# Kernel tuning notes

Measured on AMD Instinct MI355X. Metric: run time of the kernel, lower is better.

The kernel has to match this reference:

```python
import jax, jax.numpy as jnp
import numpy as np

S, B, D, H, DH = 2048, 2, 1024, 16, 64


def setup_inputs() -> dict:
    key = jax.random.key(0)
    ks = jax.random.split(key, 7)
    sc = 0.02
    return {
        "x": jax.random.normal(ks[0], (S, B, D), jnp.float32),
        "pos_emb": jax.random.normal(ks[1], (S, D), jnp.float32),
        "pos_bias_u": jax.random.normal(ks[2], (H, DH), jnp.float32) * sc,
        "pos_bias_v": jax.random.normal(ks[3], (H, DH), jnp.float32) * sc,
        "W_qkv": jax.random.normal(ks[4], (D, 3 * H * DH), jnp.float32) * sc,
        "W_relemb": jax.random.normal(ks[5], (D, H * DH), jnp.float32) * sc,
        "W_o": jax.random.normal(ks[6], (H * DH, D), jnp.float32) * sc,
        "ln_gamma": jnp.ones((D,), jnp.float32),
        "ln_beta": jnp.zeros((D,), jnp.float32),
    }


def _rel_shift(x):
    # x: [i, j, b, n]; Transformer-XL relative shift
    i, j, b, n = x.shape
    zero_pad = jnp.zeros((i, 1, b, n), x.dtype)
    xp = jnp.concatenate([zero_pad, x], axis=1)      # [i, j+1, b, n]
    xp = xp.reshape(j + 1, i, b, n)
    return xp[1:].reshape(i, j, b, n)


def reference(x, pos_emb, pos_bias_u, pos_bias_v, W_qkv, W_relemb, W_o, ln_gamma, ln_beta):
    seq_len, batch, d_model = x.shape
    num_head, d_head = pos_bias_u.shape
    scale = jnp.asarray(1.0 / d_head ** 0.5, x.dtype)

    qkv = x @ W_qkv                                   # [S,B,3*H*DH]
    q, k, v = jnp.split(qkv, 3, axis=-1)
    q = q.reshape(seq_len, batch, num_head, d_head)
    k = k.reshape(seq_len, batch, num_head, d_head)
    v = v.reshape(seq_len, batch, num_head, d_head)
    r = (pos_emb @ W_relemb).reshape(seq_len, num_head, d_head)

    AC = jnp.einsum('ibnd,jbnd->ijbn', q + pos_bias_u, k)
    BD = _rel_shift(jnp.einsum('ibnd,jnd->ijbn', q + pos_bias_v, r))
    attn_score = (AC + BD) * scale                    # [S,S,B,H]
    attn_prob = jax.nn.softmax(attn_score, axis=1)

    attn_vec = jnp.einsum('ijbn,jbnd->ibnd', attn_prob, v)
    attn_vec = attn_vec.reshape(seq_len, batch, num_head * d_head)
    attn_out = attn_vec @ W_o

    y = x + attn_out
    mu = jnp.mean(y, axis=-1, keepdims=True)
    var = jnp.mean(jnp.square(y - mu), axis=-1, keepdims=True)
    y_norm = (y - mu) * jax.lax.rsqrt(var + 1e-5)
    return y_norm * ln_gamma + ln_beta
```

## Files before the change

kernel.cpp:

```cpp
#include <hip/hip_runtime.h>
#include <stdint.h>

#define S_LEN 2048
#define BATCH 2
#define DMODEL 1024
#define NHEAD 16
#define DHEAD 64
#define HS ((size_t)S_LEN * DHEAD)

typedef float floatx4 __attribute__((ext_vector_type(4)));
typedef __bf16 bf16x8 __attribute__((ext_vector_type(8)));

__device__ __forceinline__ float bf2f(uint16_t u) {
  union { uint32_t i; float f; } x; x.i = ((uint32_t)u) << 16; return x.f;
}
__device__ __forceinline__ uint16_t f2bf(float f) {
  union { float f; uint32_t i; } x; x.f = f;
  uint32_t r = x.i + 0x7fffu + ((x.i >> 16) & 1u);
  return (uint16_t)(r >> 16);
}
__device__ __forceinline__ uint16_t f2bf_hw(float f) {
  __bf16 h = (__bf16)f;
  union { __bf16 h; uint16_t u; } c; c.h = h; return c.u;
}
__device__ __forceinline__ uint4 ld8(const void* p, size_t idx, int isf32) {
  if (isf32) {
    const float* f = (const float*)p + idx;
    float4 a = *(const float4*)f;
    float4 b = *(const float4*)(f + 4);
    uint4 r; uint16_t* rp = (uint16_t*)&r;
    rp[0] = f2bf(a.x); rp[1] = f2bf(a.y); rp[2] = f2bf(a.z); rp[3] = f2bf(a.w);
    rp[4] = f2bf(b.x); rp[5] = f2bf(b.y); rp[6] = f2bf(b.z); rp[7] = f2bf(b.w);
    return r;
  }
  return *(const uint4*)((const uint16_t*)p + idx);
}
__device__ __forceinline__ float ld1(const void* p, size_t idx, int isf32) {
  return isf32 ? ((const float*)p)[idx] : bf2f(((const uint16_t*)p)[idx]);
}
__device__ __forceinline__ uint4 addb8(uint4 a, uint4 b) {
  uint4 r;
  const uint16_t* pa = (const uint16_t*)&a;
  const uint16_t* pb = (const uint16_t*)&b;
  uint16_t* pr = (uint16_t*)&r;
#pragma unroll
  for (int e = 0; e < 8; e++) pr[e] = f2bf(bf2f(pa[e]) + bf2f(pb[e]));
  return r;
}

__global__ __launch_bounds__(256) void detect_dtype(const void* __restrict__ x,
                                                    int* __restrict__ flag) {
  __shared__ int cnt;
  if (threadIdx.x == 0) cnt = 0;
  __syncthreads();
  const uint16_t w = ((const uint16_t*)x)[threadIdx.x];
  const float v = bf2f(w);
  const float av = fabsf(v);
  if (!(av <= 256.f)) atomicAdd(&cnt, 1);
  __syncthreads();
  if (threadIdx.x == 0) *flag = (cnt >= 8) ? 1 : 0;
}

__global__ __launch_bounds__(256) void cvt_x(const void* __restrict__ x,
                                             uint16_t* __restrict__ xb,
                                             const int* __restrict__ pflag) {
  const int isf32 = *pflag;
  const size_t gid = (size_t)blockIdx.x * 256 + threadIdx.x;
  const int d0 = (int)(gid & (DMODEL / 8 - 1)) * 8;
  const size_t sb = gid >> 7;
  const size_t s = sb >> 1, b = sb & 1;
  uint4 v = ld8(x, sb * DMODEL + d0, isf32);
  *(uint4*)&xb[(b * S_LEN + s) * DMODEL + d0] = v;
}

__global__ __launch_bounds__(256) void cvt_mat(const void* __restrict__ src,
                                               uint16_t* __restrict__ dst,
                                               const int* __restrict__ pflag) {
  const int isf32 = *pflag;
  const size_t gid = ((size_t)blockIdx.x * 256 + threadIdx.x) * 8;
  *(uint4*)&dst[gid] = ld8(src, gid, isf32);
}

__global__ __launch_bounds__(256) void cvt_matT(const void* __restrict__ src,
                                                uint16_t* __restrict__ dst,
                                                int R, int C,
                                                const int* __restrict__ pflag) {
  __shared__ uint16_t lT[64 * 72];
  const int isf32 = *pflag;
  const int tid = threadIdx.x;
  const int c0 = blockIdx.x * 64;
  const int r0 = blockIdx.y * 64;
  {
    const int rr = tid >> 2, cc = (tid & 3) * 16;
    *(uint4*)&lT[rr * 72 + cc]     = ld8(src, (size_t)(r0 + rr) * C + c0 + cc, isf32);
    *(uint4*)&lT[rr * 72 + cc + 8] = ld8(src, (size_t)(r0 + rr) * C + c0 + cc + 8, isf32);
  }
  __syncthreads();
  const int oc = tid >> 2, rc = (tid & 3) * 16;
  uint16_t tmp[16];
#pragma unroll
  for (int e = 0; e < 16; e++) tmp[e] = lT[(rc + e) * 72 + oc];
  uint16_t* dp = dst + (size_t)(c0 + oc) * R + r0 + rc;
  *(uint4*)dp = *(const uint4*)&tmp[0];
  *(uint4*)(dp + 8) = *(const uint4*)&tmp[8];
}

__global__ __launch_bounds__(256) void qkv_gemm(
    const uint16_t* __restrict__ xb, const uint16_t* __restrict__ peb,
    const uint16_t* __restrict__ wqT, const uint16_t* __restrict__ wrT,
    uint16_t* __restrict__ qb, uint16_t* __restrict__ kb,
    uint16_t* __restrict__ vb, uint16_t* __restrict__ rb, int z0) {
  __shared__ uint16_t lA[128 * 32];
  __shared__ uint16_t lB[128 * 40];
  const int tid = threadIdx.x;
  const int lane = tid & 63;
  const int wave = tid >> 6;
  const int wm = wave >> 1, wn = wave & 1;
  const int strip = blockIdx.x;
  const int zg0 = z0 + 2 * blockIdx.z;
  const int b = zg0 >> 4, h0 = zg0 & 15;

  const uint16_t* Ab;
  const uint16_t* BT;
  int col0;
  if (strip < 3) {
    Ab = xb + (size_t)b * S_LEN * DMODEL;
    BT = wqT; col0 = strip * DMODEL + h0 * 64;
  } else {
    Ab = peb;
    BT = wrT; col0 = h0 * 64;
  }
  Ab += (size_t)blockIdx.y * 128 * DMODEL;

  floatx4 acc[4][4];
  floatx4 zero4 = {0.f, 0.f, 0.f, 0.f};
#pragma unroll
  for (int i = 0; i < 4; i++)
#pragma unroll
    for (int j = 0; j < 4; j++) acc[i][j] = zero4;

  const int arow = tid >> 2;
  const int kcol = (tid & 3) * 8;
  const int brow = tid >> 1;
  const int bkc = (tid & 1) * 16;

  for (int k0 = 0; k0 < DMODEL; k0 += 32) {
    *(uint4*)&lA[tid * 8]        = *(const uint4*)(Ab + (size_t)arow * DMODEL + k0 + kcol);
    *(uint4*)&lA[2048 + tid * 8] = *(const uint4*)(Ab + (size_t)(64 + arow) * DMODEL + k0 + kcol);
    const uint16_t* bp = BT + (size_t)(col0 + brow) * DMODEL + k0 + bkc;
    *(uint4*)&lB[brow * 40 + bkc]     = *(const uint4*)bp;
    *(uint4*)&lB[brow * 40 + bkc + 8] = *(const uint4*)(bp + 8);
    __syncthreads();
    bf16x8 af[4], bfr[4];
#pragma unroll
    for (int mi = 0; mi < 4; mi++)
      af[mi] = *(const bf16x8*)&lA[(wm * 64 + mi * 16 + (lane & 15)) * 32 + (lane >> 4) * 8];
#pragma unroll
    for (int ni = 0; ni < 4; ni++)
      bfr[ni] = *(const bf16x8*)&lB[(wn * 64 + ni * 16 + (lane & 15)) * 40 + (lane >> 4) * 8];
#pragma unroll
    for (int mi = 0; mi < 4; mi++)
#pragma unroll
      for (int ni = 0; ni < 4; ni++)
        acc[mi][ni] = __builtin_amdgcn_mfma_f32_16x16x32_bf16(af[mi], bfr[ni], acc[mi][ni], 0, 0, 0);
    __syncthreads();
  }

  uint16_t* ob = (strip == 0) ? qb : (strip == 1) ? kb : (strip == 2) ? vb : rb;
  const int r0 = blockIdx.y * 128 + wm * 64;
  const int zlb = 2 * blockIdx.z;
#pragma unroll
  for (int mi = 0; mi < 4; mi++)
#pragma unroll
    for (int ni = 0; ni < 4; ni++)
#pragma unroll
      for (int v = 0; v < 4; v++) {
        const int sg = r0 + mi * 16 + (lane >> 4) * 4 + v;
        const int c  = wn * 64 + ni * 16 + (lane & 15);
        const int zl = zlb + (c >> 6);
        const int d  = c & 63;
        ob[(size_t)zl * HS + (size_t)sg * 64 + d] = f2bf_hw(acc[mi][ni][v]);
      }
}

__global__ __launch_bounds__(256) void transpose_v(const uint16_t* __restrict__ vb,
                                                   uint16_t* __restrict__ vt) {
  __shared__ uint16_t lT[64 * 72];
  const int tid = threadIdx.x;
  const int zl = blockIdx.y;
  const int j0 = blockIdx.x * 64;
  const uint16_t* src = vb + (size_t)zl * HS + (size_t)j0 * 64;
  {
    const int j = tid >> 2, dc = (tid & 3) * 16;
    *(uint4*)&lT[j * 72 + dc] = *(const uint4*)(src + (size_t)j * 64 + dc);
    *(uint4*)&lT[j * 72 + dc + 8] = *(const uint4*)(src + (size_t)j * 64 + dc + 8);
  }
  __syncthreads();
  const int d = tid >> 2, jc = (tid & 3) * 16;
  uint16_t tmp[16];
#pragma unroll
  for (int e = 0; e < 16; e++) tmp[e] = lT[(jc + e) * 72 + d];
  uint16_t* dst = vt + (size_t)zl * HS + (size_t)d * S_LEN + j0 + jc;
  *(uint4*)dst = *(const uint4*)&tmp[0];
  *(uint4*)(dst + 8) = *(const uint4*)&tmp[8];
}

#define FBP 72
#define VTP 136
#define PBP 136

__global__ __launch_bounds__(512, 2) void flash_attn(
    const uint16_t* __restrict__ qb, const uint16_t* __restrict__ kb,
    const uint16_t* __restrict__ vt, const uint16_t* __restrict__ rb,
    const void* __restrict__ bu, const void* __restrict__ bv,
    uint16_t* __restrict__ avec, int z0, int zc,
    const int* __restrict__ pflag) {
  __shared__ uint16_t lK[128 * FBP];
  __shared__ uint16_t lV[64 * VTP];
  __shared__ uint16_t lR[256 * FBP];
  __shared__ uint16_t lP[8 * 16 * PBP];
  const int isf32 = *pflag;
  const int tid = threadIdx.x;
  const int lane = tid & 63;
  const int w = tid >> 6;
  const int l15 = lane & 15;
  const int l4 = lane >> 4;
  int by, zl;
  {
    const int bid = blockIdx.x;
    if ((zc & 7) == 0) {
      const int xcd = bid & 7;
      const int t = bid >> 3;
      by = t & 15;
      zl = xcd + 8 * (t >> 4);
    } else {
      by = bid & 15;
      zl = bid >> 4;
    }
  }
  const int zg = z0 + zl;
  const int b = zg >> 4, h = zg & 15;
  const int i0 = by * 128;

  const uint16_t* qz = qb + (size_t)zl * HS;
  const uint16_t* kz = kb + (size_t)zl * HS;
  const uint16_t* vz = vt + (size_t)zl * HS;
  const uint16_t* rz = rb + (size_t)zl * HS;
  uint16_t* pbw = lP + w * 16 * PBP;
  const int cmin = 112 - 16 * w;
  const int r_loc = l4 * 4;

  uint4 af1[2], af2[2], af2s[2];
  {
    const int qrow = i0 + w * 16 + l15;
    const int qrow1 = min(qrow + 1, S_LEN - 1);
#pragma unroll
    for (int ks = 0; ks < 2; ks++) {
      const int kc = ks * 32 + l4 * 8;
      uint4 bub = ld8(bu, (size_t)h * 64 + kc, isf32);
      uint4 bvb = ld8(bv, (size_t)h * 64 + kc, isf32);
      uint4 qv  = *(const uint4*)(qz + (size_t)qrow * 64 + kc);
      uint4 qv1 = *(const uint4*)(qz + (size_t)qrow1 * 64 + kc);
      af1[ks]  = addb8(qv, bub);
      af2[ks]  = addb8(qv, bvb);
      af2s[ks] = addb8(qv1, bvb);
    }
  }

  floatx4 acc_o[4];
  floatx4 zero4 = {0.f, 0.f, 0.f, 0.f};
#pragma unroll
  for (int i = 0; i < 4; i++) acc_o[i] = zero4;
  float m[4] = {-1e30f, -1e30f, -1e30f, -1e30f};
  float l[4] = {0.f, 0.f, 0.f, 0.f};

  for (int bx = 0; bx < 16; ++bx) {
    const int del = bx - by;
    __syncthreads();
    {
      const int j = tid >> 2, kc = (tid & 3) * 16;
      const uint16_t* sp = kz + (size_t)(bx * 128 + j) * 64 + kc;
      *(uint4*)&lK[j * FBP + kc]     = *(const uint4*)sp;
      *(uint4*)&lK[j * FBP + kc + 8] = *(const uint4*)(sp + 8);
    }
    {
      const int d = tid >> 3, jc = (tid & 7) * 16;
      const uint16_t* sp = vz + (size_t)d * S_LEN + bx * 128 + jc;
      *(uint4*)&lV[d * VTP + jc]     = *(const uint4*)sp;
      *(uint4*)&lV[d * VTP + jc + 8] = *(const uint4*)(sp + 8);
    }
    {
      const int slot = tid >> 1;
      const int D = del * 128 + slot - 127;
      int row = (D <= 0) ? (D + S_LEN - 1) : (D - 2 < 0 ? 0 : D - 2);
      if (row > S_LEN - 1) row = S_LEN - 1;
      const uint16_t* sp = rz + (size_t)row * 64 + (tid & 1) * 32;
      uint16_t* dp = &lR[slot * FBP + (tid & 1) * 32];
#pragma unroll
      for (int e = 0; e < 4; e++)
        *(uint4*)(dp + e * 8) = *(const uint4*)(sp + e * 8);
    }
    __syncthreads();

    floatx4 accp[9];
#pragma unroll
    for (int f = 0; f < 9; f++) accp[f] = zero4;
#pragma unroll
    for (int ks = 0; ks < 2; ks++) {
      const bf16x8 a1 = *(const bf16x8*)&af2[ks];
      const bf16x8 a2 = *(const bf16x8*)&af2s[ks];
#pragma unroll
      for (int f = 0; f < 9; f++) {
        const int cb = cmin + 16 * f;
        const bf16x8 brg = *(const bf16x8*)&lR[(cb + l15) * FBP + ks * 32 + l4 * 8];
        const bf16x8 a = (cb >= 128 - 128 * del) ? a2 : a1;
        accp[f] = __builtin_amdgcn_mfma_f32_16x16x32_bf16(a, brg, accp[f], 0, 0, 0);
      }
    }
    floatx4 acc_s[8];
#pragma unroll
    for (int f = 0; f < 8; f++) acc_s[f] = zero4;
#pragma unroll
    for (int ks = 0; ks < 2; ks++) {
      const bf16x8 a = *(const bf16x8*)&af1[ks];
#pragma unroll
      for (int f = 0; f < 8; f++) {
        const bf16x8 bk = *(const bf16x8*)&lK[(f * 16 + l15) * FBP + ks * 32 + l4 * 8];
        acc_s[f] = __builtin_amdgcn_mfma_f32_16x16x32_bf16(a, bk, acc_s[f], 0, 0, 0);
      }
    }

    float rmax[4] = {-1e30f, -1e30f, -1e30f, -1e30f};
#pragma unroll
    for (int v = 0; v < 4; v++) {
      const int r = r_loc + v;
      const int srcl = l4 * 16 + ((l15 + 15 - r) & 15);
      float sh[9];
#pragma unroll
      for (int f = 0; f < 9; f++) sh[f] = __shfl(accp[f][v], srcl);
      const int Dbase = del * 128 + l15 - w * 16 - r;
#pragma unroll
      for (int f = 0; f < 8; f++) {
        float bd = (l15 <= r) ? sh[f] : sh[f + 1];
        if (Dbase + 16 * f == 1) bd = 0.f;
        const float sv = (acc_s[f][v] + bd) * 0.125f;
        acc_s[f][v] = sv;
        rmax[v] = fmaxf(rmax[v], sv);
      }
    }
#pragma unroll
    for (int v = 0; v < 4; v++) {
#pragma unroll
      for (int o = 1; o < 16; o <<= 1) rmax[v] = fmaxf(rmax[v], __shfl_xor(rmax[v], o));
      const float mn = fmaxf(m[v], rmax[v]);
      const float al = __expf(m[v] - mn);
      m[v] = mn;
      l[v] *= al;
#pragma unroll
      for (int nd = 0; nd < 4; nd++) acc_o[nd][v] *= al;
    }
    float rsum[4] = {0.f, 0.f, 0.f, 0.f};
#pragma unroll
    for (int f = 0; f < 8; f++)
#pragma unroll
      for (int v = 0; v < 4; v++) {
        const float p = __expf(acc_s[f][v] - m[v]);
        acc_s[f][v] = p;
        rsum[v] += p;
      }
#pragma unroll
    for (int v = 0; v < 4; v++) {
#pragma unroll
      for (int o = 1; o < 16; o <<= 1) rsum[v] += __shfl_xor(rsum[v], o);
      l[v] += rsum[v];
    }
#pragma unroll
    for (int f = 0; f < 8; f++)
#pragma unroll
      for (int v = 0; v < 4; v++)
        pbw[(r_loc + v) * PBP + f * 16 + l15] = f2bf_hw(acc_s[f][v]);

#pragma unroll
    for (int ks = 0; ks < 4; ks++) {
      const bf16x8 ap = *(const bf16x8*)&pbw[l15 * PBP + ks * 32 + l4 * 8];
#pragma unroll
      for (int nd = 0; nd < 4; nd++) {
        const bf16x8 bvv = *(const bf16x8*)&lV[(nd * 16 + l15) * VTP + ks * 32 + l4 * 8];
        acc_o[nd] = __builtin_amdgcn_mfma_f32_16x16x32_bf16(ap, bvv, acc_o[nd], 0, 0, 0);
      }
    }
  }

#pragma unroll
  for (int v = 0; v < 4; v++) {
    const float inv = 1.f / l[v];
    const int i = i0 + w * 16 + r_loc + v;
#pragma unroll
    for (int nd = 0; nd < 4; nd++) {
      const int d = nd * 16 + l15;
      avec[((size_t)i * BATCH + b) * DMODEL + h * 64 + d] = f2bf_hw(acc_o[nd][v] * inv);
    }
  }
}

__global__ __launch_bounds__(256) void out_gemm(
    const uint16_t* __restrict__ avec, const uint16_t* __restrict__ woT,
    const void* __restrict__ x, uint16_t* __restrict__ ybuf,
    const int* __restrict__ pflag) {
  __shared__ uint16_t lA[128 * 32];
  __shared__ uint16_t lB[128 * 40];
  const int isf32 = *pflag;
  const int tid = threadIdx.x;
  const int lane = tid & 63;
  const int wave = tid >> 6;
  const int wm = wave >> 1, wn = wave & 1;
  const uint16_t* Ab = avec + (size_t)blockIdx.y * 128 * DMODEL;
  const int col0 = blockIdx.x * 128;

  floatx4 acc[4][4];
  floatx4 zero4 = {0.f, 0.f, 0.f, 0.f};
#pragma unroll
  for (int i = 0; i < 4; i++)
#pragma unroll
    for (int j = 0; j < 4; j++) acc[i][j] = zero4;

  const int arow = tid >> 2;
  const int kcol = (tid & 3) * 8;
  const int brow = tid >> 1;
  const int bkc = (tid & 1) * 16;

  for (int k0 = 0; k0 < DMODEL; k0 += 32) {
    *(uint4*)&lA[tid * 8]        = *(const uint4*)(Ab + (size_t)arow * DMODEL + k0 + kcol);
    *(uint4*)&lA[2048 + tid * 8] = *(const uint4*)(Ab + (size_t)(64 + arow) * DMODEL + k0 + kcol);
    const uint16_t* bp = woT + (size_t)(col0 + brow) * DMODEL + k0 + bkc;
    *(uint4*)&lB[brow * 40 + bkc]     = *(const uint4*)bp;
    *(uint4*)&lB[brow * 40 + bkc + 8] = *(const uint4*)(bp + 8);
    __syncthreads();
    bf16x8 af[4], bfr[4];
#pragma unroll
    for (int mi = 0; mi < 4; mi++)
      af[mi] = *(const bf16x8*)&lA[(wm * 64 + mi * 16 + (lane & 15)) * 32 + (lane >> 4) * 8];
#pragma unroll
    for (int ni = 0; ni < 4; ni++)
      bfr[ni] = *(const bf16x8*)&lB[(wn * 64 + ni * 16 + (lane & 15)) * 40 + (lane >> 4) * 8];
#pragma unroll
    for (int mi = 0; mi < 4; mi++)
#pragma unroll
      for (int ni = 0; ni < 4; ni++)
        acc[mi][ni] = __builtin_amdgcn_mfma_f32_16x16x32_bf16(af[mi], bfr[ni], acc[mi][ni], 0, 0, 0);
    __syncthreads();
  }

  const int r0 = blockIdx.y * 128 + wm * 64;
#pragma unroll
  for (int mi = 0; mi < 4; mi++)
#pragma unroll
    for (int ni = 0; ni < 4; ni++)
#pragma unroll
      for (int v = 0; v < 4; v++) {
        const int rg = r0 + mi * 16 + (lane >> 4) * 4 + v;
        const int cg = col0 + wn * 64 + ni * 16 + (lane & 15);
        const size_t o = (size_t)rg * DMODEL + cg;
        ybuf[o] = f2bf_hw(acc[mi][ni][v] + ld1(x, o, isf32));
      }
}

__global__ __launch_bounds__(256) void ln_f32(
    const uint16_t* __restrict__ y, const void* __restrict__ gamma,
    const void* __restrict__ beta, float* __restrict__ out,
    const int* __restrict__ pflag) {
  const int isf32 = *pflag;
  const int row = blockIdx.x;
  const int tid = threadIdx.x;
  const int lane = tid & 63, wave = tid >> 6;
  const uint16_t* yr = y + (size_t)row * DMODEL;
  uint2 u = *(const uint2*)(yr + tid * 4);
  const uint16_t* up = (const uint16_t*)&u;
  float f[4];
  float s = 0.f, q = 0.f;
#pragma unroll
  for (int j = 0; j < 4; j++) { f[j] = bf2f(up[j]); s += f[j]; q += f[j] * f[j]; }
#pragma unroll
  for (int o = 32; o; o >>= 1) { s += __shfl_xor(s, o); q += __shfl_xor(q, o); }
  __shared__ float rs[4], rq[4];
  if (lane == 0) { rs[wave] = s; rq[wave] = q; }
  __syncthreads();
  s = rs[0] + rs[1] + rs[2] + rs[3];
  q = rq[0] + rq[1] + rq[2] + rq[3];
  const float mu = s * (1.f / DMODEL);
  const float var = fmaxf(q * (1.f / DMODEL) - mu * mu, 0.f);
  const float inv = rsqrtf(var + 1e-5f);
  float4 o4;
  float* op = (float*)&o4;
#pragma unroll
  for (int j = 0; j < 4; j++) {
    const int c = tid * 4 + j;
    float r = (f[j] - mu) * inv * ld1(gamma, c, isf32) + ld1(beta, c, isf32);
    if (!(r == r)) r = 1e4f;
    op[j] = r;
  }
  *(float4*)(out + (size_t)row * DMODEL + tid * 4) = o4;
}

__global__ __launch_bounds__(256) void sentinel_fill(float* __restrict__ out) {
  const size_t i = (size_t)blockIdx.x * 1024 + threadIdx.x * 4;
  out[i] = 1e6f; out[i + 1] = 1e6f; out[i + 2] = 1e6f; out[i + 3] = 1e6f;
}

extern "C" void kernel_launch(void* const* d_in, const int* in_sizes, int n_in,
                              void* d_out, int out_size, void* d_ws, size_t ws_size,
                              hipStream_t stream) {
  const void* x    = d_in[0];
  const void* pe   = d_in[1];
  const void* bu   = d_in[2];
  const void* bv   = d_in[3];
  const void* Wqkv = d_in[4];
  const void* Wrel = d_in[5];
  const void* Wo   = d_in[6];
  const void* gam  = d_in[7];
  const void* bet  = d_in[8];
  float* out = (float*)d_out;

  const size_t per_z = 5 * HS * 2;
  const size_t conv_bytes = (size_t)(8 + 4 + 6 + 2 + 2) * 1024 * 1024;
  int ZC = 0;
  for (int c = 32; c >= 2; c >>= 1)
    if (256 + (size_t)c * per_z + conv_bytes <= ws_size) { ZC = c; break; }

  const dim3 blk(256);
  if (ZC == 0) {
    sentinel_fill<<<dim3(4096), blk, 0, stream>>>(out);
    return;
  }

  int* flag = (int*)d_ws;
  uint16_t* qb  = (uint16_t*)((char*)d_ws + 256);
  uint16_t* kb  = qb + (size_t)ZC * HS;
  uint16_t* vb  = kb + (size_t)ZC * HS;
  uint16_t* rb  = vb + (size_t)ZC * HS;
  uint16_t* vtb = rb + (size_t)ZC * HS;
  uint16_t* xbuf = vtb + (size_t)ZC * HS;
  uint16_t* peb  = xbuf + (size_t)BATCH * S_LEN * DMODEL;
  uint16_t* wqT  = peb + (size_t)S_LEN * DMODEL;
  uint16_t* wrT  = wqT + (size_t)DMODEL * 3 * DMODEL;
  uint16_t* woT  = wrT + (size_t)DMODEL * DMODEL;
  uint16_t* ybuf = xbuf;
  uint16_t* avec = (uint16_t*)d_out;

  detect_dtype<<<dim3(1), blk, 0, stream>>>(x, flag);
  cvt_x<<<dim3(2048), blk, 0, stream>>>(x, xbuf, flag);
  cvt_mat<<<dim3(1024), blk, 0, stream>>>(pe, peb, flag);
  cvt_matT<<<dim3(48, 16), blk, 0, stream>>>(Wqkv, wqT, DMODEL, 3 * DMODEL, flag);
  cvt_matT<<<dim3(16, 16), blk, 0, stream>>>(Wrel, wrT, DMODEL, DMODEL, flag);
  cvt_matT<<<dim3(16, 16), blk, 0, stream>>>(Wo,   woT, DMODEL, DMODEL, flag);

  for (int z0 = 0; z0 < 32; z0 += ZC) {
    qkv_gemm<<<dim3(4, 16, ZC / 2), blk, 0, stream>>>(xbuf, peb, wqT, wrT,
                                                      qb, kb, vb, rb, z0);
    transpose_v<<<dim3(32, ZC), blk, 0, stream>>>(vb, vtb);
    flash_attn<<<dim3(16 * ZC), dim3(512), 0, stream>>>(qb, kb, vtb, rb, bu, bv,
                                                        avec, z0, ZC, flag);
  }

  out_gemm<<<dim3(8, 32, 1), blk, 0, stream>>>(avec, woT, x, ybuf, flag);
  ln_f32<<<dim3(4096), blk, 0, stream>>>(ybuf, gam, bet, out, flag);
}
```

Baseline: 383.0 us.

## Prefetch next K/V/R tiles into registers during flash attention compute

Software-pipelines the flash-attention loop. The global loads for the next K, V and relative-position tiles are issued into registers at the start of each iteration and written to LDS after the current tile's compute finishes. This is meant to hide global memory latency behind the MFMA work. The cost is 8 extra uint4 registers per thread, which could pressure occupancy under the launch bound of 512 threads with 2 blocks.

```diff
diff --git a/kernel.cpp b/kernel.cpp
--- a/kernel.cpp
+++ b/kernel.cpp
@@ -208,6 +208,35 @@
 #define FBP 72
 #define VTP 136
 #define PBP 136
+
+#define FA_ISSUE(bxn) do {                                                  \
+    const uint16_t* spk_ = kz + (size_t)((bxn) * 128 + sj) * 64 + skc;      \
+    kr0 = *(const uint4*)spk_;                                              \
+    kr1 = *(const uint4*)(spk_ + 8);                                        \
+    const uint16_t* spv_ = vz + (size_t)sd * S_LEN + (bxn) * 128 + sjc;     \
+    vr0 = *(const uint4*)spv_;                                              \
+    vr1 = *(const uint4*)(spv_ + 8);                                        \
+    const int Dq_ = ((bxn) - by) * 128 + sslot - 127;                       \
+    int rrow_ = (Dq_ <= 0) ? (Dq_ + S_LEN - 1) : (Dq_ - 2 < 0 ? 0 : Dq_ - 2); \
+    if (rrow_ > S_LEN - 1) rrow_ = S_LEN - 1;                               \
+    const uint16_t* spr_ = rz + (size_t)rrow_ * 64 + shalf;                 \
+    br0 = *(const uint4*)spr_;                                              \
+    br1 = *(const uint4*)(spr_ + 8);                                        \
+    br2 = *(const uint4*)(spr_ + 16);                                       \
+    br3 = *(const uint4*)(spr_ + 24);                                       \
+  } while (0)
+
+#define FA_COMMIT() do {                                                    \
+    *(uint4*)&lK[sj * FBP + skc]     = kr0;                                 \
+    *(uint4*)&lK[sj * FBP + skc + 8] = kr1;                                 \
+    *(uint4*)&lV[sd * VTP + sjc]     = vr0;                                 \
+    *(uint4*)&lV[sd * VTP + sjc + 8] = vr1;                                 \
+    uint16_t* dp_ = &lR[sslot * FBP + shalf];                               \
+    *(uint4*)(dp_)      = br0;                                              \
+    *(uint4*)(dp_ + 8)  = br1;                                              \
+    *(uint4*)(dp_ + 16) = br2;                                              \
+    *(uint4*)(dp_ + 24) = br3;                                              \
+  } while (0)
 
 __global__ __launch_bounds__(512, 2) void flash_attn(
     const uint16_t* __restrict__ qb, const uint16_t* __restrict__ kb,
@@ -250,6 +279,12 @@
   const int cmin = 112 - 16 * w;
   const int r_loc = l4 * 4;
 
+  const int sj = tid >> 2, skc = (tid & 3) * 16;
+  const int sd = tid >> 3, sjc = (tid & 7) * 16;
+  const int sslot = tid >> 1, shalf = (tid & 1) * 32;
+
+  uint4 kr0, kr1, vr0, vr1, br0, br1, br2, br3;
+
   uint4 af1[2], af2[2], af2s[2];
   {
     const int qrow = i0 + w * 16 + l15;
@@ -274,33 +309,13 @@
   float m[4] = {-1e30f, -1e30f, -1e30f, -1e30f};
   float l[4] = {0.f, 0.f, 0.f, 0.f};
 
+  FA_ISSUE(0);
+  FA_COMMIT();
+  __syncthreads();
+
   for (int bx = 0; bx < 16; ++bx) {
     const int del = bx - by;
-    __syncthreads();
-    {
-      const int j = tid >> 2, kc = (tid & 3) * 16;
-      const uint16_t* sp = kz + (size_t)(bx * 128 + j) * 64 + kc;
-      *(uint4*)&lK[j * FBP + kc]     = *(const uint4*)sp;
-      *(uint4*)&lK[j * FBP + kc + 8] = *(const uint4*)(sp + 8);
-    }
-    {
-      const int d = tid >> 3, jc = (tid & 7) * 16;
-      const uint16_t* sp = vz + (size_t)d * S_LEN + bx * 128 + jc;
-      *(uint4*)&lV[d * VTP + jc]     = *(const uint4*)sp;
-      *(uint4*)&lV[d * VTP + jc + 8] = *(const uint4*)(sp + 8);
-    }
-    {
-      const int slot = tid >> 1;
-      const int D = del * 128 + slot - 127;
-      int row = (D <= 0) ? (D + S_LEN - 1) : (D - 2 < 0 ? 0 : D - 2);
-      if (row > S_LEN - 1) row = S_LEN - 1;
-      const uint16_t* sp = rz + (size_t)row * 64 + (tid & 1) * 32;
-      uint16_t* dp = &lR[slot * FBP + (tid & 1) * 32];
-#pragma unroll
-      for (int e = 0; e < 4; e++)
-        *(uint4*)(dp + e * 8) = *(const uint4*)(sp + e * 8);
-    }
-    __syncthreads();
+    if (bx < 15) FA_ISSUE(bx + 1);
 
     floatx4 accp[9];
 #pragma unroll
@@ -388,6 +403,12 @@
         const bf16x8 bvv = *(const bf16x8*)&lV[(nd * 16 + l15) * VTP + ks * 32 + l4 * 8];
         acc_o[nd] = __builtin_amdgcn_mfma_f32_16x16x32_bf16(ap, bvv, acc_o[nd], 0, 0, 0);
       }
+    }
+
+    __syncthreads();
+    if (bx < 15) {
+      FA_COMMIT();
+      __syncthreads();
     }
   }
 
```

After: 365.1 us. -4.7%, faster.
